# Kernel tuning notes

Measured on AMD Instinct MI355X. Metric: run time of the kernel, lower is better.

The kernel has to match this reference:

```python
import jax, jax.numpy as jnp
import numpy as np

N, G, H1, H2, HEADS, EMB, C, S = 4096, 2048, 512, 128, 8, 16, 20, 4
CH = H1 // HEADS  # per-head channels = 64
EPS = 1e-6
COEF_FE = 0.1


def _uni(k, shape, fan_in, fan_out):
    c = np.sqrt(6.0 / (fan_in + fan_out)).astype(np.float32)
    return jax.random.uniform(k, shape, jnp.float32, -c, c)


def setup_inputs() -> dict:
    key = jax.random.key(0)
    ks = jax.random.split(key, 40)
    adj = (jax.random.uniform(ks[0], (N, N)) < 0.005).astype(jnp.float32)
    adj = jnp.maximum(adj, jnp.eye(N, dtype=jnp.float32))  # self-loops, no empty rows
    node_feats = jax.random.normal(ks[1], (N, G), jnp.float32)
    count_matrix = jax.random.randint(ks[2], (N, G), 0, 50).astype(jnp.float32)
    library_size = jax.random.uniform(ks[3], (N, 1), jnp.float32, 0.5, 2.0)
    slice_label = jax.random.randint(ks[4], (N,), 0, S)
    basis = jax.random.uniform(ks[5], (C, G), jnp.float32)
    # encoder GAT layer1: HEADS heads, c_in=G -> c_out=CH each
    We1 = _uni(ks[6], (HEADS, CH, G), G, CH)
    be1 = jnp.zeros((HEADS, CH), jnp.float32)
    v0e1 = _uni(ks[7], (HEADS, CH, 1), CH, 1)
    v1e1 = _uni(ks[8], (HEADS, CH, 1), CH, 1)
    # encoder dense layer2: H1 -> H2
    W2 = _uni(ks[9], (H2, H1), H1, H2)
    b2 = jnp.zeros((H2,), jnp.float32)
    # decoder GAT layer1: c_in = H2+EMB -> CH per head
    CIN_D = H2 + EMB
    Wd1 = _uni(ks[10], (HEADS, CH, CIN_D), CIN_D, CH)
    bd1 = jnp.zeros((HEADS, CH), jnp.float32)
    v0d1 = _uni(ks[11], (HEADS, CH, 1), CH, 1)
    v1d1 = _uni(ks[12], (HEADS, CH, 1), CH, 1)
    # decoder dense layer2: H1 -> G
    Wd2 = _uni(ks[13], (G, H1), H1, G)
    bd2 = jnp.zeros((G,), jnp.float32)
    # deconv alpha (H2+EMB -> 1) and beta (H2 -> C); zero-init in torch, small random here
    Wa = 0.01 * jax.random.normal(ks[14], (1, CIN_D), jnp.float32)
    ba = jnp.zeros((1,), jnp.float32)
    Wb = 0.01 * jax.random.normal(ks[15], (C, H2), jnp.float32)
    bb = jnp.zeros((C,), jnp.float32)
    gamma = 0.01 * jax.random.normal(ks[16], (S, G), jnp.float32)
    logtheta = 5.0 * jnp.ones((S, G), jnp.float32)
    emb_table = jax.random.normal(ks[17], (S, EMB), jnp.float32)
    return dict(adj_matrix=adj, node_feats=node_feats, count_matrix=count_matrix,
                library_size=library_size, slice_label=slice_label, basis=basis,
                We1=We1, be1=be1, v0e1=v0e1, v1e1=v1e1, W2=W2, b2=b2,
                Wd1=Wd1, bd1=bd1, v0d1=v0d1, v1d1=v1d1, Wd2=Wd2, bd2=bd2,
                Wa=Wa, ba=ba, Wb=Wb, bb=bb, gamma=gamma, logtheta=logtheta,
                emb_table=emb_table)


def _gat_head(x, adj, W, b, v0, v1):
    h = x @ W.T + b                       # [N, CH]
    logits = adj * ((h @ v0) + (h @ v1).T)  # [N, N]; zero where adj==0
    s = jax.nn.sigmoid(logits) - 0.5       # unnormalized attentions
    mask = adj != 0.0
    e = jnp.where(mask, jnp.exp(s), 0.0)    # sparse softmax over structural nonzeros (temp=1)
    den = e.sum(axis=1, keepdims=True)
    p = e / jnp.where(den == 0.0, 1.0, den)
    return p @ h                            # [N, CH]


def _gat_multi(x, adj, Ws, bs, v0s, v1s):
    return jnp.concatenate([_gat_head(x, adj, Ws[i], bs[i], v0s[i], v1s[i])
                            for i in range(HEADS)], axis=1)


def reference(adj_matrix, node_feats, count_matrix, library_size, slice_label, basis,
              We1, be1, v0e1, v1e1, W2, b2, Wd1, bd1, v0d1, v1d1, Wd2, bd2,
              Wa, ba, Wb, bb, gamma, logtheta, emb_table):
    # encoder
    H = jax.nn.elu(_gat_multi(node_feats, adj_matrix, We1, be1, v0e1, v1e1))
    Z = H @ W2.T + b2                                   # [N, H2]
    emb = emb_table[slice_label]                        # [N, EMB]
    # deconvolutioner
    beta = jax.nn.softmax(jax.nn.elu(Z) @ Wb.T + bb, axis=1)   # [N, C]
    Hc = jax.nn.elu(jnp.concatenate([Z, emb], axis=1))
    alpha = Hc @ Wa.T + ba                              # [N, 1]
    # decoder
    Hd = jax.nn.elu(_gat_multi(jnp.concatenate([Z, emb], axis=1), adj_matrix,
                               Wd1, bd1, v0d1, v1d1))
    X_recon = Hd @ Wd2.T + bd2                          # [N, G]
    features_loss = jnp.mean(jnp.sqrt(jnp.sum((node_feats - X_recon) ** 2, axis=1)))
    # NB deconvolution loss
    log_lam = jnp.log(beta @ basis + EPS) + alpha + gamma[slice_label]
    lam = jnp.exp(log_lam)
    th = jnp.exp(logtheta)[slice_label]                 # [N, G]
    mu = library_size * lam
    ll = (jax.lax.lgamma(count_matrix + th + EPS) - jax.lax.lgamma(th + EPS)
          + th * jnp.log(th + EPS) - th * jnp.log(th + mu + EPS)
          + count_matrix * jnp.log(mu + EPS) - count_matrix * jnp.log(th + mu + EPS))
    decon_loss = -jnp.mean(jnp.sum(ll, axis=1))
    return decon_loss + COEF_FE * features_loss
```

## Files before the change

kernel.cpp:

```cpp
#include <hip/hip_runtime.h>
#include <hip/hip_bf16.h>
#include <math.h>

#define N 4096
#define G 2048
#define H1 512
#define H2 128
#define HEADS 8
#define EMB 16
#define C 20
#define S 4
#define CH 64
#define CIN_D (H2 + EMB)
#define KD_PAD 160
#define KB_PAD 32
#define CAP 128
#define EPSV 1e-6f

typedef __attribute__((ext_vector_type(8))) short short8;
typedef __attribute__((ext_vector_type(8))) short bf16x8;
typedef __attribute__((ext_vector_type(4))) float f32x4;

__device__ __forceinline__ unsigned short f2b(float x) {
    __hip_bfloat16 h = __float2bfloat16(x);
    return *reinterpret_cast<unsigned short*>(&h);
}
__device__ __forceinline__ float b2f(unsigned short u) {
    unsigned int x = ((unsigned int)u) << 16;
    return __uint_as_float(x);
}
__device__ __forceinline__ float lgamma_fast(float x) {
    float sh = 0.f;
    while (x < 8.f) { sh -= __logf(x); x += 1.f; }
    float ix = 1.f / x;
    float lx = __logf(x);
    return (x - 0.5f) * lx - x + 0.91893853f
         + ix * (0.08333333f - 0.00277778f * ix * ix) + sh;
}

__global__ void build_csr(const float* __restrict__ adj, int* __restrict__ col_idx,
                          int* __restrict__ row_cnt) {
    int i = blockIdx.x;
    int lane = threadIdx.x;
    int cnt = 0;
    const float4* row4 = (const float4*)(adj + (size_t)i * N);
    int* cols = col_idx + (size_t)i * CAP;
    unsigned long long lmask = (1ull << lane) - 1ull;
    for (int c = 0; c < N / 256; ++c) {
        float4 v = row4[c * 64 + lane];
        float vv[4] = {v.x, v.y, v.z, v.w};
        #pragma unroll
        for (int s = 0; s < 4; ++s) {
            unsigned long long m = __ballot(vv[s] != 0.f);
            if (vv[s] != 0.f) {
                int idx = cnt + __popcll(m & lmask);
                if (idx < CAP) cols[idx] = c * 256 + lane * 4 + s;
            }
            cnt += __popcll(m);
        }
    }
    if (lane == 0) row_cnt[i] = cnt < CAP ? cnt : CAP;
}

__global__ void f2bf_vec(const float* __restrict__ in, unsigned short* __restrict__ out, int n4) {
    int i = blockIdx.x * 256 + threadIdx.x;
    if (i >= n4) return;
    float4 v = ((const float4*)in)[i];
    ushort4 o;
    o.x = f2b(v.x); o.y = f2b(v.y); o.z = f2b(v.z); o.w = f2b(v.w);
    ((ushort4*)out)[i] = o;
}

__global__ void convert_wd1(const float* __restrict__ in, unsigned short* __restrict__ out) {
    int idx = blockIdx.x * 256 + threadIdx.x;
    if (idx >= H1 * KD_PAD) return;
    int n = idx / KD_PAD, k = idx - n * KD_PAD;
    out[idx] = f2b(k < CIN_D ? in[n * CIN_D + k] : 0.f);
}

__global__ void convert_basisT(const float* __restrict__ basis, unsigned short* __restrict__ out) {
    int idx = blockIdx.x * 256 + threadIdx.x;
    if (idx >= G * KB_PAD) return;
    int g = idx >> 5, c = idx & 31;
    out[idx] = f2b(c < C ? basis[c * G + g] : 0.f);
}

#define LDP 40
template<int FM, int OBF, int KS>
__global__ __launch_bounds__(256) void gemm_mfma(const unsigned short* __restrict__ A,
                                                 const unsigned short* __restrict__ B,
                                                 const float* __restrict__ bias,
                                                 void* __restrict__ Cout,
                                                 int M, int Nc, int K) {
    constexpr int BMT = FM * 32;
    __shared__ short As[BMT * LDP];
    __shared__ short Bs[128 * LDP];
    int bn = blockIdx.x, bm = blockIdx.y;
    int kz = (KS > 1) ? blockIdx.z : 0;
    int t = threadIdx.x;
    int lane = t & 63, wid = t >> 6;
    int wr = wid >> 1, wc = wid & 1;
    f32x4 acc[FM][4] = {};
    const short* Ag = (const short*)A + (size_t)(bm * BMT) * K;
    const short* Bg = (const short*)B + (size_t)(bn * 128) * K;
    int r0 = t >> 2, q0 = t & 3;
    int rbase = (lane & 15);
    int koff = (lane >> 4) * 8;
    int kbeg = kz * (K / KS), kend = kbeg + K / KS;

    for (int k0 = kbeg; k0 < kend; k0 += 32) {
        short8 a0 = *(const short8*)(Ag + (size_t)r0 * K + k0 + q0 * 8);
        short8 a1;
        if constexpr (FM == 4) a1 = *(const short8*)(Ag + (size_t)(r0 + 64) * K + k0 + q0 * 8);
        short8 b0 = *(const short8*)(Bg + (size_t)r0 * K + k0 + q0 * 8);
        short8 b1 = *(const short8*)(Bg + (size_t)(r0 + 64) * K + k0 + q0 * 8);
        __syncthreads();
        *(short8*)(As + r0 * LDP + q0 * 8) = a0;
        if constexpr (FM == 4) *(short8*)(As + (r0 + 64) * LDP + q0 * 8) = a1;
        *(short8*)(Bs + r0 * LDP + q0 * 8) = b0;
        *(short8*)(Bs + (r0 + 64) * LDP + q0 * 8) = b1;
        __syncthreads();
        bf16x8 af[FM], bfr[4];
        #pragma unroll
        for (int m = 0; m < FM; ++m)
            af[m] = *(const bf16x8*)(As + (wr * FM * 16 + m * 16 + rbase) * LDP + koff);
        #pragma unroll
        for (int n = 0; n < 4; ++n)
            bfr[n] = *(const bf16x8*)(Bs + (wc * 64 + n * 16 + rbase) * LDP + koff);
        #pragma unroll
        for (int m = 0; m < FM; ++m)
            #pragma unroll
            for (int n = 0; n < 4; ++n)
                acc[m][n] = __builtin_amdgcn_mfma_f32_16x16x32_bf16(af[m], bfr[n], acc[m][n], 0, 0, 0);
    }
    int colb = bn * 128 + wc * 64;
    int rowb = bm * BMT + wr * FM * 16;
    #pragma unroll
    for (int m = 0; m < FM; ++m) {
        #pragma unroll
        for (int n = 0; n < 4; ++n) {
            int col = colb + n * 16 + (lane & 15);
            int row0 = rowb + m * 16 + (lane >> 4) * 4;
            if constexpr (KS > 1) {
                float* Cp = (float*)Cout + (size_t)kz * M * Nc;
                #pragma unroll
                for (int r = 0; r < 4; ++r)
                    Cp[(size_t)(row0 + r) * Nc + col] = acc[m][n][r];
            } else {
                float bs = bias ? bias[col] : 0.f;
                #pragma unroll
                for (int r = 0; r < 4; ++r) {
                    float v = acc[m][n][r] + bs;
                    if constexpr (OBF)
                        ((unsigned short*)Cout)[(size_t)(row0 + r) * Nc + col] = f2b(v);
                    else
                        ((float*)Cout)[(size_t)(row0 + r) * Nc + col] = v;
                }
            }
        }
    }
}

template<int KS, int OBF>
__global__ __launch_bounds__(256) void reduce_k(const float* __restrict__ Cp,
                                                const float* __restrict__ bias,
                                                void* __restrict__ out,
                                                int total4, int ncmask) {
    int i = blockIdx.x * 256 + threadIdx.x;
    if (i >= total4) return;
    float4 s = ((const float4*)Cp)[i];
    #pragma unroll
    for (int ks = 1; ks < KS; ++ks) {
        float4 v = ((const float4*)(Cp + (size_t)ks * total4 * 4))[i];
        s.x += v.x; s.y += v.y; s.z += v.z; s.w += v.w;
    }
    int col = (i * 4) & ncmask;
    s.x += bias[col]; s.y += bias[col + 1]; s.z += bias[col + 2]; s.w += bias[col + 3];
    if constexpr (OBF) {
        ushort4 o;
        o.x = f2b(s.x); o.y = f2b(s.y); o.z = f2b(s.z); o.w = f2b(s.w);
        ((ushort4*)out)[i] = o;
    } else {
        ((float4*)out)[i] = s;
    }
}

__global__ __launch_bounds__(256) void gemm_recon_sq(const unsigned short* __restrict__ A,
                                                     const unsigned short* __restrict__ B,
                                                     const float* __restrict__ bias,
                                                     const unsigned short* __restrict__ nfb,
                                                     float* __restrict__ sq_part) {
    constexpr int K = H1;
    __shared__ short As[128 * LDP];
    __shared__ short Bs[128 * LDP];
    __shared__ float red[4][64];
    int bn = blockIdx.x, bm = blockIdx.y;
    int t = threadIdx.x;
    int lane = t & 63, wid = t >> 6;
    int wr = wid >> 1, wc = wid & 1;
    f32x4 acc[4][4] = {};
    const short* Ag = (const short*)A + (size_t)(bm * 128) * K;
    const short* Bg = (const short*)B + (size_t)(bn * 128) * K;
    int r0 = t >> 2, q0 = t & 3;
    int rbase = (lane & 15);
    int koff = (lane >> 4) * 8;

    for (int k0 = 0; k0 < K; k0 += 32) {
        short8 a0 = *(const short8*)(Ag + (size_t)r0 * K + k0 + q0 * 8);
        short8 a1 = *(const short8*)(Ag + (size_t)(r0 + 64) * K + k0 + q0 * 8);
        short8 b0 = *(const short8*)(Bg + (size_t)r0 * K + k0 + q0 * 8);
        short8 b1 = *(const short8*)(Bg + (size_t)(r0 + 64) * K + k0 + q0 * 8);
        __syncthreads();
        *(short8*)(As + r0 * LDP + q0 * 8) = a0;
        *(short8*)(As + (r0 + 64) * LDP + q0 * 8) = a1;
        *(short8*)(Bs + r0 * LDP + q0 * 8) = b0;
        *(short8*)(Bs + (r0 + 64) * LDP + q0 * 8) = b1;
        __syncthreads();
        bf16x8 af[4], bfr[4];
        #pragma unroll
        for (int m = 0; m < 4; ++m)
            af[m] = *(const bf16x8*)(As + (wr * 64 + m * 16 + rbase) * LDP + koff);
        #pragma unroll
        for (int n = 0; n < 4; ++n)
            bfr[n] = *(const bf16x8*)(Bs + (wc * 64 + n * 16 + rbase) * LDP + koff);
        #pragma unroll
        for (int m = 0; m < 4; ++m)
            #pragma unroll
            for (int n = 0; n < 4; ++n)
                acc[m][n] = __builtin_amdgcn_mfma_f32_16x16x32_bf16(af[m], bfr[n], acc[m][n], 0, 0, 0);
    }
    int colb = bn * 128 + wc * 64;
    int rowb = bm * 128 + wr * 64;
    float part[4][4];
    #pragma unroll
    for (int m = 0; m < 4; ++m) {
        #pragma unroll
        for (int r = 0; r < 4; ++r) part[m][r] = 0.f;
        #pragma unroll
        for (int n = 0; n < 4; ++n) {
            int col = colb + n * 16 + (lane & 15);
            float bs = bias[col];
            int row0 = rowb + m * 16 + (lane >> 4) * 4;
            #pragma unroll
            for (int r = 0; r < 4; ++r) {
                float d = b2f(nfb[(size_t)(row0 + r) * G + col]) - (acc[m][n][r] + bs);
                part[m][r] += d * d;
            }
        }
    }
    #pragma unroll
    for (int m = 0; m < 4; ++m)
        #pragma unroll
        for (int r = 0; r < 4; ++r) {
            float v = part[m][r];
            v += __shfl_xor(v, 1); v += __shfl_xor(v, 2);
            v += __shfl_xor(v, 4); v += __shfl_xor(v, 8);
            part[m][r] = v;
        }
    if ((lane & 15) == 0) {
        int q = lane >> 4;
        #pragma unroll
        for (int m = 0; m < 4; ++m)
            #pragma unroll
            for (int r = 0; r < 4; ++r)
                red[wid][m * 16 + q * 4 + r] = part[m][r];
    }
    __syncthreads();
    if (t < 128) {
        int wr2 = t >> 6, loc = t & 63;
        float v = red[wr2 * 2 + 0][loc] + red[wr2 * 2 + 1][loc];
        sq_part[(size_t)(bm * 128 + t) * 16 + bn] = v;
    }
}

__global__ __launch_bounds__(256) void nb_loss_ew(const float* __restrict__ BD,
                                                  const float* __restrict__ cm,
                                                  const int* __restrict__ slab,
                                                  const float* __restrict__ muf,
                                                  const float* __restrict__ kco,
                                                  const float* __restrict__ th_a,
                                                  const float* __restrict__ eg_a,
                                                  const float* __restrict__ gm_a,
                                                  const float* __restrict__ ax_a,
                                                  float* __restrict__ ll_row) {
    int row = blockIdx.x * 4 + (threadIdx.x >> 6);
    int lane = threadIdx.x & 63;
    int sl = slab[row];
    float mufv = muf[row], kcov = kco[row];
    const float* bdr = BD + (size_t)row * G;
    const float* cmr = cm + (size_t)row * G;
    size_t sgb = (size_t)sl * G;
    float acc = 0.f;
    #pragma unroll 2
    for (int it = 0; it < G / 256; ++it) {
        int c = it * 256 + lane * 4;
        f32x4 bd4 = *(const f32x4*)(bdr + c);
        f32x4 k4  = *(const f32x4*)(cmr + c);
        f32x4 th4 = *(const f32x4*)(th_a + sgb + c);
        f32x4 eg4 = *(const f32x4*)(eg_a + sgb + c);
        f32x4 gm4 = *(const f32x4*)(gm_a + sgb + c);
        f32x4 ax4 = *(const f32x4*)(ax_a + sgb + c);
        #pragma unroll
        for (int j = 0; j < 4; ++j) {
            float th = th4[j], k = k4[j];
            float ebd = bd4[j] + EPSV;
            float lbd = __logf(ebd);
            float mu = mufv * ebd * eg4[j];
            float lgx = lgamma_fast(k + th + EPSV);
            acc += lgx + ax4[j] - (th + k) * __logf(th + mu + EPSV)
                 + k * (kcov + lbd + gm4[j]);
        }
    }
    #pragma unroll
    for (int m = 32; m; m >>= 1) acc += __shfl_xor(acc, m);
    if (lane == 0) ll_row[row] = acc;
}

__global__ void head_dots(const unsigned short* __restrict__ Hb, const float* __restrict__ v0,
                          const float* __restrict__ v1, float* __restrict__ hv0,
                          float* __restrict__ hv1) {
    int i = blockIdx.x;
    int lane = threadIdx.x;
    #pragma unroll
    for (int h = 0; h < HEADS; ++h) {
        float v = b2f(Hb[(size_t)i * H1 + h * CH + lane]);
        float p0 = v * v0[h * CH + lane];
        float p1 = v * v1[h * CH + lane];
        #pragma unroll
        for (int m = 32; m; m >>= 1) {
            p0 += __shfl_xor(p0, m);
            p1 += __shfl_xor(p1, m);
        }
        if (lane == 0) {
            hv0[i * HEADS + h] = p0;
            hv1[i * HEADS + h] = p1;
        }
    }
}

__global__ void edge_weights(const float* __restrict__ hv0, const float* __restrict__ hv1,
                             const int* __restrict__ col_idx, const int* __restrict__ row_cnt,
                             float* __restrict__ ew) {
    int i = blockIdx.x;
    int lane = threadIdx.x;
    int cnt = row_cnt[i];
    const int* cols = col_idx + (size_t)i * CAP;
    int e0 = lane, e1 = lane + 64;
    int j0 = (e0 < cnt) ? cols[e0] : 0;
    int j1 = (e1 < cnt) ? cols[e1] : 0;
    #pragma unroll
    for (int h = 0; h < HEADS; ++h) {
        float a0 = hv0[i * HEADS + h];
        float w0 = 0.f, w1 = 0.f;
        if (e0 < cnt) {
            float x = a0 + hv1[j0 * HEADS + h];
            w0 = __expf(1.f / (1.f + __expf(-x)) - 0.5f);
        }
        if (e1 < cnt) {
            float x = a0 + hv1[j1 * HEADS + h];
            w1 = __expf(1.f / (1.f + __expf(-x)) - 0.5f);
        }
        float den = w0 + w1;
        #pragma unroll
        for (int m = 32; m; m >>= 1) den += __shfl_xor(den, m);
        float inv = 1.f / den;
        if (e0 < cnt) ew[((size_t)i * CAP + e0) * HEADS + h] = w0 * inv;
        if (e1 < cnt) ew[((size_t)i * CAP + e1) * HEADS + h] = w1 * inv;
    }
}

__global__ __launch_bounds__(512) void attn_agg2(const unsigned short* __restrict__ Hb,
                                                 const float* __restrict__ ew,
                                                 const int* __restrict__ col_idx,
                                                 const int* __restrict__ row_cnt,
                                                 unsigned short* __restrict__ out) {
    __shared__ float red[8][64 * 8];
    int i = blockIdx.x;
    int t = threadIdx.x;
    int slot = t >> 6;
    int cg = t & 63;
    int h = cg >> 3;
    int cnt = row_cnt[i];
    const int* cols = col_idx + (size_t)i * CAP;
    float acc[8];
    #pragma unroll
    for (int k = 0; k < 8; ++k) acc[k] = 0.f;
    for (int e = slot; e < cnt; e += 8) {
        int j = cols[e];
        float wv = ew[((size_t)i * CAP + e) * HEADS + h];
        short8 hv = ((const short8*)(Hb + (size_t)j * H1))[cg];
        #pragma unroll
        for (int k = 0; k < 8; ++k)
            acc[k] += wv * b2f((unsigned short)hv[k]);
    }
    #pragma unroll
    for (int k = 0; k < 8; ++k) red[slot][cg * 8 + k] = acc[k];
    __syncthreads();
    if (slot < 4) {
        #pragma unroll
        for (int k = 0; k < 8; ++k) red[slot][cg * 8 + k] += red[slot + 4][cg * 8 + k];
    }
    __syncthreads();
    if (slot < 2) {
        #pragma unroll
        for (int k = 0; k < 8; ++k) red[slot][cg * 8 + k] += red[slot + 2][cg * 8 + k];
    }
    __syncthreads();
    if (slot == 0) {
        short8 o;
        #pragma unroll
        for (int k = 0; k < 8; ++k) {
            float v = red[0][cg * 8 + k] + red[1][cg * 8 + k];
            v = (v > 0.f) ? v : expm1f(v);
            o[k] = (short)f2b(v);
        }
        ((short8*)(out + (size_t)i * H1))[cg] = o;
    }
}

__global__ void pernode(const float* __restrict__ Z, const float* __restrict__ emb_table,
                        const int* __restrict__ slab, const float* __restrict__ Wb,
                        const float* __restrict__ bb, const float* __restrict__ Wa,
                        const float* __restrict__ ba, const float* __restrict__ lib,
                        unsigned short* __restrict__ beta_bf, float* __restrict__ muf,
                        float* __restrict__ kco, unsigned short* __restrict__ Xdb) {
    int i = blockIdx.x;
    int lane = threadIdx.x;
    __shared__ float sZ[H2];
    __shared__ float sE[EMB];
    __shared__ float sLog[C];
    __shared__ float sAl;
    sZ[lane] = Z[(size_t)i * H2 + lane];
    sZ[64 + lane] = Z[(size_t)i * H2 + 64 + lane];
    int s = slab[i];
    if (lane < EMB) sE[lane] = emb_table[s * EMB + lane];
    __syncthreads();
    Xdb[(size_t)i * KD_PAD + lane] = f2b(sZ[lane]);
    Xdb[(size_t)i * KD_PAD + 64 + lane] = f2b(sZ[64 + lane]);
    if (lane < EMB) Xdb[(size_t)i * KD_PAD + H2 + lane] = f2b(sE[lane]);
    if (lane < KD_PAD - CIN_D) Xdb[(size_t)i * KD_PAD + CIN_D + lane] = 0;
    if (lane < C) {
        float acc = bb[lane];
        for (int k = 0; k < H2; ++k) {
            float z = sZ[k];
            float e = z > 0.f ? z : expm1f(z);
            acc += e * Wb[lane * H2 + k];
        }
        sLog[lane] = acc;
    }
    __syncthreads();
    if (lane == 0) {
        float mx = sLog[0];
        for (int c = 1; c < C; ++c) mx = fmaxf(mx, sLog[c]);
        float sm = 0.f;
        for (int c = 0; c < C; ++c) { float e = __expf(sLog[c] - mx); sLog[c] = e; sm += e; }
        for (int c = 0; c < C; ++c) sLog[c] /= sm;
    }
    __syncthreads();
    if (lane < KB_PAD) beta_bf[(size_t)i * KB_PAD + lane] = (lane < C) ? f2b(sLog[lane]) : 0;
    float x0 = sZ[lane];        x0 = x0 > 0.f ? x0 : expm1f(x0);
    float x1 = sZ[64 + lane];   x1 = x1 > 0.f ? x1 : expm1f(x1);
    float p = x0 * Wa[lane] + x1 * Wa[64 + lane];
    if (lane < EMB) {
        float x2 = sE[lane];    x2 = x2 > 0.f ? x2 : expm1f(x2);
        p += x2 * Wa[H2 + lane];
    }
    #pragma unroll
    for (int m = 32; m; m >>= 1) p += __shfl_xor(p, m);
    if (lane == 0) sAl = p + ba[0];
    __syncthreads();
    if (lane == 0) {
        float A = sAl, L = lib[i];
        muf[i] = L * __expf(A);
        kco[i] = __logf(L) + A;
    }
}

__global__ void theta_tables(const float* __restrict__ logtheta, const float* __restrict__ gamma,
                             float* __restrict__ th_a, float* __restrict__ eg_a,
                             float* __restrict__ gm_a, float* __restrict__ ax_a) {
    int idx = blockIdx.x * 256 + threadIdx.x;
    if (idx >= S * G) return;
    float th = __expf(logtheta[idx]);
    float gm = gamma[idx];
    th_a[idx] = th;
    eg_a[idx] = __expf(gm);
    gm_a[idx] = gm;
    ax_a[idx] = th * __logf(th + EPSV) - lgammaf(th + EPSV);
}

__global__ void row_reduce(const float* __restrict__ ll_row, const float* __restrict__ sq_part,
                           float* __restrict__ part_ll, float* __restrict__ part_sq) {
    int blk = blockIdx.x, lane = threadIdx.x;
    int row = blk * 64 + lane;
    float s1 = ll_row[row];
    float s2 = 0.f;
    #pragma unroll
    for (int j = 0; j < 16; ++j) s2 += sq_part[(size_t)row * 16 + j];
    float b = sqrtf(s2);
    #pragma unroll
    for (int m = 32; m; m >>= 1) { s1 += __shfl_xor(s1, m); b += __shfl_xor(b, m); }
    if (lane == 0) { part_ll[blk] = s1; part_sq[blk] = b; }
}

__global__ void finalize2(const float* __restrict__ part_ll, const float* __restrict__ part_sq,
                          float* __restrict__ out) {
    int lane = threadIdx.x;
    float a = part_ll[lane], b = part_sq[lane];
    #pragma unroll
    for (int m = 32; m; m >>= 1) { a += __shfl_xor(a, m); b += __shfl_xor(b, m); }
    if (lane == 0) out[0] = -(a / (float)N) + 0.1f * (b / (float)N);
}

extern "C" void kernel_launch(void* const* d_in, const int* in_sizes, int n_in,
                              void* d_out, int out_size, void* d_ws, size_t ws_size,
                              hipStream_t stream) {
    const float* adj       = (const float*)d_in[0];
    const float* node_f    = (const float*)d_in[1];
    const float* count_m   = (const float*)d_in[2];
    const float* lib       = (const float*)d_in[3];
    const int*   slab      = (const int*)d_in[4];
    const float* basis     = (const float*)d_in[5];
    const float* We1       = (const float*)d_in[6];
    const float* be1       = (const float*)d_in[7];
    const float* v0e1      = (const float*)d_in[8];
    const float* v1e1      = (const float*)d_in[9];
    const float* W2        = (const float*)d_in[10];
    const float* b2        = (const float*)d_in[11];
    const float* Wd1       = (const float*)d_in[12];
    const float* bd1       = (const float*)d_in[13];
    const float* v0d1      = (const float*)d_in[14];
    const float* v1d1      = (const float*)d_in[15];
    const float* Wd2       = (const float*)d_in[16];
    const float* bd2       = (const float*)d_in[17];
    const float* Wa        = (const float*)d_in[18];
    const float* ba        = (const float*)d_in[19];
    const float* Wb        = (const float*)d_in[20];
    const float* bb        = (const float*)d_in[21];
    const float* gamma     = (const float*)d_in[22];
    const float* logtheta  = (const float*)d_in[23];
    const float* emb_table = (const float*)d_in[24];
    float* out = (float*)d_out;

    char* w = (char*)d_ws;
    auto alloc = [&](size_t bytes) { void* p = (void*)w; w += (bytes + 255) & ~(size_t)255; return p; };
    int*   col_idx = (int*)  alloc((size_t)N * CAP * 4);
    int*   row_cnt = (int*)  alloc((size_t)N * 4);
    unsigned short* Hlin_bf = (unsigned short*)alloc((size_t)N * H1 * 2);
    unsigned short* Hgat_bf = (unsigned short*)alloc((size_t)N * H1 * 2);
    float* Z       = (float*)alloc((size_t)N * H2 * 4);
    unsigned short* Xd_bf   = (unsigned short*)alloc((size_t)N * KD_PAD * 2);
    unsigned short* beta_bf = (unsigned short*)alloc((size_t)N * KB_PAD * 2);
    float* muf     = (float*)alloc((size_t)N * 4);
    float* kco     = (float*)alloc((size_t)N * 4);
    float* hv0     = (float*)alloc((size_t)N * HEADS * 4);
    float* hv1     = (float*)alloc((size_t)N * HEADS * 4);
    float* ew      = (float*)alloc((size_t)N * CAP * HEADS * 4);
    float* th_a    = (float*)alloc((size_t)S * G * 4);
    float* eg_a    = (float*)alloc((size_t)S * G * 4);
    float* gm_a    = (float*)alloc((size_t)S * G * 4);
    float* ax_a    = (float*)alloc((size_t)S * G * 4);
    float* Cp      = (float*)alloc((size_t)4 * N * H1 * 4);
    float* BD      = (float*)alloc((size_t)N * G * 4);
    float* ll_row  = (float*)alloc((size_t)N * 4);
    float* sq_part = (float*)alloc((size_t)N * 16 * 4);
    float* part_ll = (float*)alloc(64 * 4);
    float* part_sq = (float*)alloc(64 * 4);
    unsigned short* nf_bf    = (unsigned short*)alloc((size_t)N * G * 2);
    unsigned short* We1_bf   = (unsigned short*)alloc((size_t)H1 * G * 2);
    unsigned short* W2_bf    = (unsigned short*)alloc((size_t)H2 * H1 * 2);
    unsigned short* Wd1_bf   = (unsigned short*)alloc((size_t)H1 * KD_PAD * 2);
    unsigned short* Wd2_bf   = (unsigned short*)alloc((size_t)G * H1 * 2);
    unsigned short* basisT_bf= (unsigned short*)alloc((size_t)G * KB_PAD * 2);

    build_csr<<<dim3(N), dim3(64), 0, stream>>>(adj, col_idx, row_cnt);
    theta_tables<<<dim3((S * G + 255) / 256), dim3(256), 0, stream>>>(
        logtheta, gamma, th_a, eg_a, gm_a, ax_a);
    f2bf_vec<<<dim3((N * G / 4 + 255) / 256), dim3(256), 0, stream>>>(node_f, nf_bf, N * G / 4);
    f2bf_vec<<<dim3((H1 * G / 4 + 255) / 256), dim3(256), 0, stream>>>(We1, We1_bf, H1 * G / 4);
    f2bf_vec<<<dim3((H2 * H1 / 4 + 255) / 256), dim3(256), 0, stream>>>(W2, W2_bf, H2 * H1 / 4);
    convert_wd1<<<dim3((H1 * KD_PAD + 255) / 256), dim3(256), 0, stream>>>(Wd1, Wd1_bf);
    f2bf_vec<<<dim3((G * H1 / 4 + 255) / 256), dim3(256), 0, stream>>>(Wd2, Wd2_bf, G * H1 / 4);
    convert_basisT<<<dim3((G * KB_PAD + 255) / 256), dim3(256), 0, stream>>>(basis, basisT_bf);

    gemm_mfma<2, 0, 4><<<dim3(H1 / 128, N / 64, 4), dim3(256), 0, stream>>>(
        nf_bf, We1_bf, be1, Cp, N, H1, G);
    reduce_k<4, 1><<<dim3((N * H1 / 4 + 255) / 256), dim3(256), 0, stream>>>(
        Cp, be1, Hlin_bf, N * H1 / 4, H1 - 1);
    head_dots<<<dim3(N), dim3(64), 0, stream>>>(Hlin_bf, v0e1, v1e1, hv0, hv1);
    edge_weights<<<dim3(N), dim3(64), 0, stream>>>(hv0, hv1, col_idx, row_cnt, ew);
    attn_agg2<<<dim3(N), dim3(512), 0, stream>>>(Hlin_bf, ew, col_idx, row_cnt, Hgat_bf);
    gemm_mfma<2, 0, 8><<<dim3(H2 / 128, N / 64, 8), dim3(256), 0, stream>>>(
        Hgat_bf, W2_bf, b2, Cp, N, H2, H1);
    reduce_k<8, 0><<<dim3((N * H2 / 4 + 255) / 256), dim3(256), 0, stream>>>(
        Cp, b2, Z, N * H2 / 4, H2 - 1);
    pernode<<<dim3(N), dim3(64), 0, stream>>>(Z, emb_table, slab, Wb, bb, Wa, ba, lib,
                                              beta_bf, muf, kco, Xd_bf);
    gemm_mfma<2, 0, 1><<<dim3(G / 128, N / 64), dim3(256), 0, stream>>>(
        beta_bf, basisT_bf, nullptr, BD, N, G, KB_PAD);
    nb_loss_ew<<<dim3(N / 4), dim3(256), 0, stream>>>(
        BD, count_m, slab, muf, kco, th_a, eg_a, gm_a, ax_a, ll_row);
    gemm_mfma<2, 1, 1><<<dim3(H1 / 128, N / 64), dim3(256), 0, stream>>>(
        Xd_bf, Wd1_bf, bd1, Hlin_bf, N, H1, KD_PAD);
    head_dots<<<dim3(N), dim3(64), 0, stream>>>(Hlin_bf, v0d1, v1d1, hv0, hv1);
    edge_weights<<<dim3(N), dim3(64), 0, stream>>>(hv0, hv1, col_idx, row_cnt, ew);
    attn_agg2<<<dim3(N), dim3(512), 0, stream>>>(Hlin_bf, ew, col_idx, row_cnt, Hgat_bf);
    gemm_recon_sq<<<dim3(G / 128, N / 128), dim3(256), 0, stream>>>(
        Hgat_bf, Wd2_bf, bd2, nf_bf, sq_part);
    row_reduce<<<dim3(64), dim3(64), 0, stream>>>(ll_row, sq_part, part_ll, part_sq);
    finalize2<<<dim3(1), dim3(64), 0, stream>>>(part_ll, part_sq, out);
}
```

Measured before the change: 221.3 us.

## Fuse prep conversions, fuse edge weights into attention, store BD as bf16

Merges the theta-table and all fp32-to-bf16 conversion kernels into a single segmented prep launch. Folds the edge_weights kernel into the attention aggregation kernel, which now computes the per-edge weights and softmax denominators in shared memory, so the large per-edge weight buffer is never written to or read from global memory. The beta@basis GEMM now writes bf16 instead of fp32, halving that intermediate's traffic, at some cost in precision inside the log. It also halves the row tile of the reconstruction GEMM to 64 to launch more blocks.

Measured after the change: 201.7 us. 1.1x faster.

```diff
diff --git a/kernel.cpp b/kernel.cpp
--- a/kernel.cpp
+++ b/kernel.cpp
@@ -62,27 +62,68 @@
     if (lane == 0) row_cnt[i] = cnt < CAP ? cnt : CAP;
 }
 
-__global__ void f2bf_vec(const float* __restrict__ in, unsigned short* __restrict__ out, int n4) {
-    int i = blockIdx.x * 256 + threadIdx.x;
-    if (i >= n4) return;
+#define SEG_SG   (S * G)
+#define SEG_NF4  (N * G / 4)
+#define SEG_WE4  (H1 * G / 4)
+#define SEG_W24  (H2 * H1 / 4)
+#define SEG_WD1E (H1 * KD_PAD)
+#define SEG_WD24 (G * H1 / 4)
+#define SEG_BTE  (G * KB_PAD)
+#define PREP_TOTAL (SEG_SG + SEG_NF4 + SEG_WE4 + SEG_W24 + SEG_WD1E + SEG_WD24 + SEG_BTE)
+
+__device__ __forceinline__ void cvt4(const float* __restrict__ in,
+                                     unsigned short* __restrict__ out, int i) {
     float4 v = ((const float4*)in)[i];
     ushort4 o;
     o.x = f2b(v.x); o.y = f2b(v.y); o.z = f2b(v.z); o.w = f2b(v.w);
     ((ushort4*)out)[i] = o;
 }
 
-__global__ void convert_wd1(const float* __restrict__ in, unsigned short* __restrict__ out) {
+__global__ __launch_bounds__(256) void prep(const float* __restrict__ logtheta,
+                                            const float* __restrict__ gamma,
+                                            float* __restrict__ th_a, float* __restrict__ eg_a,
+                                            float* __restrict__ gm_a, float* __restrict__ ax_a,
+                                            const float* __restrict__ node_f,
+                                            unsigned short* __restrict__ nf_bf,
+                                            const float* __restrict__ We1,
+                                            unsigned short* __restrict__ We1_bf,
+                                            const float* __restrict__ W2,
+                                            unsigned short* __restrict__ W2_bf,
+                                            const float* __restrict__ Wd1,
+                                            unsigned short* __restrict__ Wd1_bf,
+                                            const float* __restrict__ Wd2,
+                                            unsigned short* __restrict__ Wd2_bf,
+                                            const float* __restrict__ basis,
+                                            unsigned short* __restrict__ basisT_bf) {
     int idx = blockIdx.x * 256 + threadIdx.x;
-    if (idx >= H1 * KD_PAD) return;
-    int n = idx / KD_PAD, k = idx - n * KD_PAD;
-    out[idx] = f2b(k < CIN_D ? in[n * CIN_D + k] : 0.f);
-}
-
-__global__ void convert_basisT(const float* __restrict__ basis, unsigned short* __restrict__ out) {
-    int idx = blockIdx.x * 256 + threadIdx.x;
-    if (idx >= G * KB_PAD) return;
-    int g = idx >> 5, c = idx & 31;
-    out[idx] = f2b(c < C ? basis[c * G + g] : 0.f);
+    if (idx < SEG_SG) {
+        float th = __expf(logtheta[idx]);
+        float gm = gamma[idx];
+        th_a[idx] = th;
+        eg_a[idx] = __expf(gm);
+        gm_a[idx] = gm;
+        ax_a[idx] = th * __logf(th + EPSV) - lgammaf(th + EPSV);
+        return;
+    }
+    idx -= SEG_SG;
+    if (idx < SEG_NF4) { cvt4(node_f, nf_bf, idx); return; }
+    idx -= SEG_NF4;
+    if (idx < SEG_WE4) { cvt4(We1, We1_bf, idx); return; }
+    idx -= SEG_WE4;
+    if (idx < SEG_W24) { cvt4(W2, W2_bf, idx); return; }
+    idx -= SEG_W24;
+    if (idx < SEG_WD1E) {
+        int n = idx / KD_PAD, k = idx - n * KD_PAD;
+        Wd1_bf[idx] = f2b(k < CIN_D ? Wd1[n * CIN_D + k] : 0.f);
+        return;
+    }
+    idx -= SEG_WD1E;
+    if (idx < SEG_WD24) { cvt4(Wd2, Wd2_bf, idx); return; }
+    idx -= SEG_WD24;
+    if (idx < SEG_BTE) {
+        int g = idx >> 5, c = idx & 31;
+        basisT_bf[idx] = f2b(c < C ? basis[c * G + g] : 0.f);
+    }
 }
 
 #define LDP 40
@@ -191,15 +232,15 @@
                                                      const unsigned short* __restrict__ nfb,
                                                      float* __restrict__ sq_part) {
     constexpr int K = H1;
-    __shared__ short As[128 * LDP];
+    __shared__ short As[64 * LDP];
     __shared__ short Bs[128 * LDP];
-    __shared__ float red[4][64];
+    __shared__ float red[4][32];
     int bn = blockIdx.x, bm = blockIdx.y;
     int t = threadIdx.x;
     int lane = t & 63, wid = t >> 6;
     int wr = wid >> 1, wc = wid & 1;
-    f32x4 acc[4][4] = {};
-    const short* Ag = (const short*)A + (size_t)(bm * 128) * K;
+    f32x4 acc[2][4] = {};
+    const short* Ag = (const short*)A + (size_t)(bm * 64) * K;
     const short* Bg = (const short*)B + (size_t)(bn * 128) * K;
     int r0 = t >> 2, q0 = t & 3;
     int rbase = (lane & 15);
@@ -207,33 +248,31 @@
 
     for (int k0 = 0; k0 < K; k0 += 32) {
         short8 a0 = *(const short8*)(Ag + (size_t)r0 * K + k0 + q0 * 8);
-        short8 a1 = *(const short8*)(Ag + (size_t)(r0 + 64) * K + k0 + q0 * 8);
         short8 b0 = *(const short8*)(Bg + (size_t)r0 * K + k0 + q0 * 8);
         short8 b1 = *(const short8*)(Bg + (size_t)(r0 + 64) * K + k0 + q0 * 8);
         __syncthreads();
         *(short8*)(As + r0 * LDP + q0 * 8) = a0;
-        *(short8*)(As + (r0 + 64) * LDP + q0 * 8) = a1;
         *(short8*)(Bs + r0 * LDP + q0 * 8) = b0;
         *(short8*)(Bs + (r0 + 64) * LDP + q0 * 8) = b1;
         __syncthreads();
-        bf16x8 af[4], bfr[4];
-        #pragma unroll
-        for (int m = 0; m < 4; ++m)
-            af[m] = *(const bf16x8*)(As + (wr * 64 + m * 16 + rbase) * LDP + koff);
+        bf16x8 af[2], bfr[4];
+        #pragma unroll
+        for (int m = 0; m < 2; ++m)
+            af[m] = *(const bf16x8*)(As + (wr * 32 + m * 16 + rbase) * LDP + koff);
         #pragma unroll
         for (int n = 0; n < 4; ++n)
             bfr[n] = *(const bf16x8*)(Bs + (wc * 64 + n * 16 + rbase) * LDP + koff);
         #pragma unroll
-        for (int m = 0; m < 4; ++m)
+        for (int m = 0; m < 2; ++m)
             #pragma unroll
             for (int n = 0; n < 4; ++n)
                 acc[m][n] = __builtin_amdgcn_mfma_f32_16x16x32_bf16(af[m], bfr[n], acc[m][n], 0, 0, 0);
     }
     int colb = bn * 128 + wc * 64;
-    int rowb = bm * 128 + wr * 64;
-    float part[4][4];
-    #pragma unroll
-    for (int m = 0; m < 4; ++m) {
+    int rowb = bm * 64 + wr * 32;
+    float part[2][4];
+    #pragma unroll
+    for (int m = 0; m < 2; ++m) {
         #pragma unroll
         for (int r = 0; r < 4; ++r) part[m][r] = 0.f;
         #pragma unroll
@@ -249,7 +288,7 @@
         }
     }
     #pragma unroll
-    for (int m = 0; m < 4; ++m)
+    for (int m = 0; m < 2; ++m)
         #pragma unroll
         for (int r = 0; r < 4; ++r) {
             float v = part[m][r];
@@ -260,20 +299,20 @@
     if ((lane & 15) == 0) {
         int q = lane >> 4;
         #pragma unroll
-        for (int m = 0; m < 4; ++m)
+        for (int m = 0; m < 2; ++m)
             #pragma unroll
             for (int r = 0; r < 4; ++r)
                 red[wid][m * 16 + q * 4 + r] = part[m][r];
     }
     __syncthreads();
-    if (t < 128) {
-        int wr2 = t >> 6, loc = t & 63;
+    if (t < 64) {
+        int wr2 = t >> 5, loc = t & 31;
         float v = red[wr2 * 2 + 0][loc] + red[wr2 * 2 + 1][loc];
-        sq_part[(size_t)(bm * 128 + t) * 16 + bn] = v;
-    }
-}
-
-__global__ __launch_bounds__(256) void nb_loss_ew(const float* __restrict__ BD,
+        sq_part[(size_t)(bm * 64 + t) * 16 + bn] = v;
+    }
+}
+
+__global__ __launch_bounds__(256) void nb_loss_ew(const unsigned short* __restrict__ BDb,
                                                   const float* __restrict__ cm,
                                                   const int* __restrict__ slab,
                                                   const float* __restrict__ muf,
@@ -287,23 +326,24 @@
     int lane = threadIdx.x & 63;
     int sl = slab[row];
     float mufv = muf[row], kcov = kco[row];
-    const float* bdr = BD + (size_t)row * G;
+    const unsigned short* bdr = BDb + (size_t)row * G;
     const float* cmr = cm + (size_t)row * G;
     size_t sgb = (size_t)sl * G;
     float acc = 0.f;
     #pragma unroll 2
     for (int it = 0; it < G / 256; ++it) {
         int c = it * 256 + lane * 4;
-        f32x4 bd4 = *(const f32x4*)(bdr + c);
+        ushort4 bdu = *(const ushort4*)(bdr + c);
         f32x4 k4  = *(const f32x4*)(cmr + c);
         f32x4 th4 = *(const f32x4*)(th_a + sgb + c);
         f32x4 eg4 = *(const f32x4*)(eg_a + sgb + c);
         f32x4 gm4 = *(const f32x4*)(gm_a + sgb + c);
         f32x4 ax4 = *(const f32x4*)(ax_a + sgb + c);
+        float bdv[4] = {b2f(bdu.x), b2f(bdu.y), b2f(bdu.z), b2f(bdu.w)};
         #pragma unroll
         for (int j = 0; j < 4; ++j) {
             float th = th4[j], k = k4[j];
-            float ebd = bd4[j] + EPSV;
+            float ebd = bdv[j] + EPSV;
             float lbd = __logf(ebd);
             float mu = mufv * ebd * eg4[j];
             float lgx = lgamma_fast(k + th + EPSV);
@@ -338,56 +378,45 @@
     }
 }
 
-__global__ void edge_weights(const float* __restrict__ hv0, const float* __restrict__ hv1,
-                             const int* __restrict__ col_idx, const int* __restrict__ row_cnt,
-                             float* __restrict__ ew) {
-    int i = blockIdx.x;
-    int lane = threadIdx.x;
-    int cnt = row_cnt[i];
-    const int* cols = col_idx + (size_t)i * CAP;
-    int e0 = lane, e1 = lane + 64;
-    int j0 = (e0 < cnt) ? cols[e0] : 0;
-    int j1 = (e1 < cnt) ? cols[e1] : 0;
-    #pragma unroll
-    for (int h = 0; h < HEADS; ++h) {
-        float a0 = hv0[i * HEADS + h];
-        float w0 = 0.f, w1 = 0.f;
-        if (e0 < cnt) {
-            float x = a0 + hv1[j0 * HEADS + h];
-            w0 = __expf(1.f / (1.f + __expf(-x)) - 0.5f);
-        }
-        if (e1 < cnt) {
-            float x = a0 + hv1[j1 * HEADS + h];
-            w1 = __expf(1.f / (1.f + __expf(-x)) - 0.5f);
-        }
-        float den = w0 + w1;
-        #pragma unroll
-        for (int m = 32; m; m >>= 1) den += __shfl_xor(den, m);
-        float inv = 1.f / den;
-        if (e0 < cnt) ew[((size_t)i * CAP + e0) * HEADS + h] = w0 * inv;
-        if (e1 < cnt) ew[((size_t)i * CAP + e1) * HEADS + h] = w1 * inv;
-    }
-}
-
-__global__ __launch_bounds__(512) void attn_agg2(const unsigned short* __restrict__ Hb,
-                                                 const float* __restrict__ ew,
-                                                 const int* __restrict__ col_idx,
-                                                 const int* __restrict__ row_cnt,
-                                                 unsigned short* __restrict__ out) {
+__global__ __launch_bounds__(512) void attn_fused(const unsigned short* __restrict__ Hb,
+                                                  const float* __restrict__ hv0,
+                                                  const float* __restrict__ hv1,
+                                                  const int* __restrict__ col_idx,
+                                                  const int* __restrict__ row_cnt,
+                                                  unsigned short* __restrict__ out) {
+    __shared__ int scols[CAP];
+    __shared__ float sw[CAP][HEADS];
+    __shared__ float sden[HEADS];
     __shared__ float red[8][64 * 8];
     int i = blockIdx.x;
     int t = threadIdx.x;
+    int cnt = row_cnt[i];
+    const int* cols = col_idx + (size_t)i * CAP;
+    if (t < cnt) scols[t] = cols[t];
+    __syncthreads();
+    for (int idx = t; idx < cnt * HEADS; idx += 512) {
+        int e = idx >> 3, h = idx & 7;
+        int j = scols[e];
+        float x = hv0[i * HEADS + h] + hv1[j * HEADS + h];
+        sw[e][h] = __expf(1.f / (1.f + __expf(-x)) - 0.5f);
+    }
+    __syncthreads();
+    if (t < HEADS) {
+        float d = 0.f;
+        for (int e = 0; e < cnt; ++e) d += sw[e][t];
+        sden[t] = 1.f / d;
+    }
+    __syncthreads();
     int slot = t >> 6;
     int cg = t & 63;
     int h = cg >> 3;
-    int cnt = row_cnt[i];
-    const int* cols = col_idx + (size_t)i * CAP;
+    float inv = sden[h];
     float acc[8];
     #pragma unroll
     for (int k = 0; k < 8; ++k) acc[k] = 0.f;
     for (int e = slot; e < cnt; e += 8) {
-        int j = cols[e];
-        float wv = ew[((size_t)i * CAP + e) * HEADS + h];
+        int j = scols[e];
+        float wv = sw[e][h] * inv;
         short8 hv = ((const short8*)(Hb + (size_t)j * H1))[cg];
         #pragma unroll
         for (int k = 0; k < 8; ++k)
@@ -474,19 +503,6 @@
         muf[i] = L * __expf(A);
         kco[i] = __logf(L) + A;
     }
-}
-
-__global__ void theta_tables(const float* __restrict__ logtheta, const float* __restrict__ gamma,
-                             float* __restrict__ th_a, float* __restrict__ eg_a,
-                             float* __restrict__ gm_a, float* __restrict__ ax_a) {
-    int idx = blockIdx.x * 256 + threadIdx.x;
-    if (idx >= S * G) return;
-    float th = __expf(logtheta[idx]);
-    float gm = gamma[idx];
-    th_a[idx] = th;
-    eg_a[idx] = __expf(gm);
-    gm_a[idx] = gm;
-    ax_a[idx] = th * __logf(th + EPSV) - lgammaf(th + EPSV);
 }
 
 __global__ void row_reduce(const float* __restrict__ ll_row, const float* __restrict__ sq_part,
@@ -555,13 +571,12 @@
     float* kco     = (float*)alloc((size_t)N * 4);
     float* hv0     = (float*)alloc((size_t)N * HEADS * 4);
     float* hv1     = (float*)alloc((size_t)N * HEADS * 4);
-    float* ew      = (float*)alloc((size_t)N * CAP * HEADS * 4);
     float* th_a    = (float*)alloc((size_t)S * G * 4);
     float* eg_a    = (float*)alloc((size_t)S * G * 4);
     float* gm_a    = (float*)alloc((size_t)S * G * 4);
     float* ax_a    = (float*)alloc((size_t)S * G * 4);
     float* Cp      = (float*)alloc((size_t)4 * N * H1 * 4);
-    float* BD      = (float*)alloc((size_t)N * G * 4);
+    unsigned short* BDb = (unsigned short*)alloc((size_t)N * G * 2);
     float* ll_row  = (float*)alloc((size_t)N * 4);
     float* sq_part = (float*)alloc((size_t)N * 16 * 4);
     float* part_ll = (float*)alloc(64 * 4);
@@ -574,38 +589,31 @@
     unsigned short* basisT_bf= (unsigned short*)alloc((size_t)G * KB_PAD * 2);
 
     build_csr<<<dim3(N), dim3(64), 0, stream>>>(adj, col_idx, row_cnt);
-    theta_tables<<<dim3((S * G + 255) / 256), dim3(256), 0, stream>>>(
-        logtheta, gamma, th_a, eg_a, gm_a, ax_a);
-    f2bf_vec<<<dim3((N * G / 4 + 255) / 256), dim3(256), 0, stream>>>(node_f, nf_bf, N * G / 4);
-    f2bf_vec<<<dim3((H1 * G / 4 + 255) / 256), dim3(256), 0, stream>>>(We1, We1_bf, H1 * G / 4);
-    f2bf_vec<<<dim3((H2 * H1 / 4 + 255) / 256), dim3(256), 0, stream>>>(W2, W2_bf, H2 * H1 / 4);
-    convert_wd1<<<dim3((H1 * KD_PAD + 255) / 256), dim3(256), 0, stream>>>(Wd1, Wd1_bf);
-    f2bf_vec<<<dim3((G * H1 / 4 + 255) / 256), dim3(256), 0, stream>>>(Wd2, Wd2_bf, G * H1 / 4);
-    convert_basisT<<<dim3((G * KB_PAD + 255) / 256), dim3(256), 0, stream>>>(basis, basisT_bf);
+    prep<<<dim3(PREP_TOTAL / 256), dim3(256), 0, stream>>>(
+        logtheta, gamma, th_a, eg_a, gm_a, ax_a,
+        node_f, nf_bf, We1, We1_bf, W2, W2_bf, Wd1, Wd1_bf, Wd2, Wd2_bf, basis, basisT_bf);
 
     gemm_mfma<2, 0, 4><<<dim3(H1 / 128, N / 64, 4), dim3(256), 0, stream>>>(
         nf_bf, We1_bf, be1, Cp, N, H1, G);
     reduce_k<4, 1><<<dim3((N * H1 / 4 + 255) / 256), dim3(256), 0, stream>>>(
         Cp, be1, Hlin_bf, N * H1 / 4, H1 - 1);
     head_dots<<<dim3(N), dim3(64), 0, stream>>>(Hlin_bf, v0e1, v1e1, hv0, hv1);
-    edge_weights<<<dim3(N), dim3(64), 0, stream>>>(hv0, hv1, col_idx, row_cnt, ew);
-    attn_agg2<<<dim3(N), dim3(512), 0, stream>>>(Hlin_bf, ew, col_idx, row_cnt, Hgat_bf);
+    attn_fused<<<dim3(N), dim3(512), 0, stream>>>(Hlin_bf, hv0, hv1, col_idx, row_cnt, Hgat_bf);
     gemm_mfma<2, 0, 8><<<dim3(H2 / 128, N / 64, 8), dim3(256), 0, stream>>>(
         Hgat_bf, W2_bf, b2, Cp, N, H2, H1);
     reduce_k<8, 0><<<dim3((N * H2 / 4 + 255) / 256), dim3(256), 0, stream>>>(
         Cp, b2, Z, N * H2 / 4, H2 - 1);
     pernode<<<dim3(N), dim3(64), 0, stream>>>(Z, emb_table, slab, Wb, bb, Wa, ba, lib,
                                               beta_bf, muf, kco, Xd_bf);
-    gemm_mfma<2, 0, 1><<<dim3(G / 128, N / 64), dim3(256), 0, stream>>>(
-        beta_bf, basisT_bf, nullptr, BD, N, G, KB_PAD);
+    gemm_mfma<2, 1, 1><<<dim3(G / 128, N / 64), dim3(256), 0, stream>>>(
+        beta_bf, basisT_bf, nullptr, BDb, N, G, KB_PAD);
     nb_loss_ew<<<dim3(N / 4), dim3(256), 0, stream>>>(
-        BD, count_m, slab, muf, kco, th_a, eg_a, gm_a, ax_a, ll_row);
+        BDb, count_m, slab, muf, kco, th_a, eg_a, gm_a, ax_a, ll_row);
     gemm_mfma<2, 1, 1><<<dim3(H1 / 128, N / 64), dim3(256), 0, stream>>>(
         Xd_bf, Wd1_bf, bd1, Hlin_bf, N, H1, KD_PAD);
     head_dots<<<dim3(N), dim3(64), 0, stream>>>(Hlin_bf, v0d1, v1d1, hv0, hv1);
-    edge_weights<<<dim3(N), dim3(64), 0, stream>>>(hv0, hv1, col_idx, row_cnt, ew);
-    attn_agg2<<<dim3(N), dim3(512), 0, stream>>>(Hlin_bf, ew, col_idx, row_cnt, Hgat_bf);
-    gemm_recon_sq<<<dim3(G / 128, N / 128), dim3(256), 0, stream>>>(
+    attn_fused<<<dim3(N), dim3(512), 0, stream>>>(Hlin_bf, hv0, hv1, col_idx, row_cnt, Hgat_bf);
+    gemm_recon_sq<<<dim3(G / 128, N / 64), dim3(256), 0, stream>>>(
         Hgat_bf, Wd2_bf, bd2, nf_bf, sq_part);
     row_reduce<<<dim3(64), dim3(64), 0, stream>>>(ll_row, sq_part, part_ll, part_sq);
     finalize2<<<dim3(1), dim3(64), 0, stream>>>(part_ll, part_sq, out);
```
